# Kernel tuning notes

Measured on AMD Instinct MI355X. Metric: run time of the kernel, lower is better.

## Reference

```python
import jax, jax.numpy as jnp
import numpy as np

N_ITEMS = 100000
HIDDEN = 128
N_EDGES = 1600000


def setup_inputs() -> dict:
    key = jax.random.key(0)
    k1, k2, k3, k4 = jax.random.split(key, 4)
    item_emb = jax.random.normal(k1, (N_ITEMS, HIDDEN), dtype=jnp.float32) * 0.02
    adj_rows = jax.random.randint(k2, (N_EDGES,), 0, N_ITEMS, dtype=jnp.int32)
    adj_cols = jax.random.randint(k3, (N_EDGES,), 0, N_ITEMS, dtype=jnp.int32)
    adj_vals = jax.random.uniform(k4, (N_EDGES,), dtype=jnp.float32)
    return {
        "item_emb": item_emb,
        "adj_rows": adj_rows,
        "adj_cols": adj_cols,
        "adj_vals": adj_vals,
        "num_layers": 3,
    }


def _spmm(rows, cols, vals, embeds, n_rows):
    # y[r] = sum_{e: rows[e]==r} vals[e] * embeds[cols[e]]  (COO spmm)
    gathered = embeds[cols] * vals[:, None]  # [E, H]
    return jax.ops.segment_sum(gathered, rows, num_segments=n_rows)


def reference(item_emb, adj_rows, adj_cols, adj_vals, num_layers):
    embeds = [item_emb]
    for _ in range(num_layers):
        embeds.append(_spmm(adj_rows, adj_cols, adj_vals, embeds[-1], item_emb.shape[0]))
    # sum over all layer embeddings (running-sum aggregation)
    total = embeds[0]
    for e in embeds[1:]:
        total = total + e
    return (total, jnp.stack(embeds, axis=0))
```

## Files before the change

### kernel.cpp

```cpp
#include <hip/hip_runtime.h>
#include <hip/hip_fp16.h>

#define HIDDEN 128
#define SCAN_TILE 1024
#define SCAN_BLOCK 256

__global__ void zero_counts(int* __restrict__ counts, int n) {
    int i = blockIdx.x * blockDim.x + threadIdx.x;
    int stride = gridDim.x * blockDim.x;
    for (; i < n; i += stride) counts[i] = 0;
}

__global__ void hist_kernel(const int* __restrict__ rows, int* __restrict__ counts, int E) {
    int i = blockIdx.x * blockDim.x + threadIdx.x;
    int stride = gridDim.x * blockDim.x;
    for (; i < E; i += stride) atomicAdd(&counts[rows[i]], 1);
}

__global__ void scan_partial_sums(const int* __restrict__ counts,
                                  int* __restrict__ block_sums,
                                  int n) {
    __shared__ int sdata[SCAN_BLOCK];
    int t = threadIdx.x;
    int idx = blockIdx.x * SCAN_TILE + t * 4;
    int s = 0;
    if (idx + 3 < n) {
        int4 c = *reinterpret_cast<const int4*>(counts + idx);
        s = c.x + c.y + c.z + c.w;
    } else if (idx < n) {
        s = counts[idx];
        if (idx + 1 < n) s += counts[idx + 1];
        if (idx + 2 < n) s += counts[idx + 2];
    }
    sdata[t] = s;
    __syncthreads();
    for (int off = SCAN_BLOCK / 2; off > 0; off >>= 1) {
        if (t < off) sdata[t] += sdata[t + off];
        __syncthreads();
    }
    if (t == 0) block_sums[blockIdx.x] = sdata[0];
}

__global__ void scan_block_offsets(int* __restrict__ block_sums,
                                   int* __restrict__ row_ptr,
                                   int nb, int n) {
    __shared__ int sdata[SCAN_BLOCK];
    int t = threadIdx.x;
    int chunk = (nb + SCAN_BLOCK - 1) / SCAN_BLOCK;
    int lo = t * chunk;
    int hi = min(lo + chunk, nb);
    int s = 0;
    for (int i = lo; i < hi; ++i) s += block_sums[i];
    sdata[t] = s;
    __syncthreads();
    for (int off = 1; off < SCAN_BLOCK; off <<= 1) {
        int u = (t >= off) ? sdata[t - off] : 0;
        __syncthreads();
        sdata[t] += u;
        __syncthreads();
    }
    int run = sdata[t] - s;
    for (int i = lo; i < hi; ++i) {
        int v = block_sums[i];
        block_sums[i] = run;
        run += v;
    }
    if (t == SCAN_BLOCK - 1) row_ptr[n] = sdata[SCAN_BLOCK - 1];
}

__global__ void scan_apply(const int* counts,
                           const int* __restrict__ block_offsets,
                           int* __restrict__ row_ptr,
                           int* cursor,
                           int n) {
    __shared__ int sdata[SCAN_BLOCK];
    int t = threadIdx.x;
    int idx = blockIdx.x * SCAN_TILE + t * 4;
    int v0 = 0, v1 = 0, v2 = 0, v3 = 0;
    if (idx + 3 < n) {
        int4 c = *reinterpret_cast<const int4*>(counts + idx);
        v0 = c.x; v1 = c.y; v2 = c.z; v3 = c.w;
    } else if (idx < n) {
        v0 = counts[idx];
        if (idx + 1 < n) v1 = counts[idx + 1];
        if (idx + 2 < n) v2 = counts[idx + 2];
    }
    int s = v0 + v1 + v2 + v3;
    sdata[t] = s;
    __syncthreads();
    for (int off = 1; off < SCAN_BLOCK; off <<= 1) {
        int u = (t >= off) ? sdata[t - off] : 0;
        __syncthreads();
        sdata[t] += u;
        __syncthreads();
    }
    int run = sdata[t] - s + block_offsets[blockIdx.x];
    if (idx < n)     { row_ptr[idx]     = run; cursor[idx]     = run; run += v0; }
    if (idx + 1 < n) { row_ptr[idx + 1] = run; cursor[idx + 1] = run; run += v1; }
    if (idx + 2 < n) { row_ptr[idx + 2] = run; cursor[idx + 2] = run; run += v2; }
    if (idx + 3 < n) { row_ptr[idx + 3] = run; cursor[idx + 3] = run; run += v3; }
}

__global__ void scatter_kernel(const int* __restrict__ rows,
                               const int* __restrict__ cols,
                               const float* __restrict__ vals,
                               int* __restrict__ cursor,
                               int2* __restrict__ colval,
                               int E) {
    int i = blockIdx.x * blockDim.x + threadIdx.x;
    int stride = gridDim.x * blockDim.x;
    for (; i < E; i += stride) {
        int r = rows[i];
        int pos = atomicAdd(&cursor[r], 1);
        colval[pos] = make_int2(cols[i], __float_as_int(vals[i]));
    }
}

__global__ void convert_copy(const float4* __restrict__ src,
                             float4* __restrict__ s0,
                             float4* __restrict__ xh,
                             size_t n8) {
    size_t stride = (size_t)gridDim.x * blockDim.x;
    for (size_t i = (size_t)blockIdx.x * blockDim.x + threadIdx.x; i < n8; i += stride) {
        float4 a = src[i * 2];
        float4 b = src[i * 2 + 1];
        s0[i * 2]     = a;
        s0[i * 2 + 1] = b;
        __half2 h[4];
        h[0] = __floats2half2_rn(a.x, a.y);
        h[1] = __floats2half2_rn(a.z, a.w);
        h[2] = __floats2half2_rn(b.x, b.y);
        h[3] = __floats2half2_rn(b.z, b.w);
        xh[i] = *reinterpret_cast<float4*>(h);
    }
}

template <bool WRITE_SHADOW>
__global__ void spmm_h16(const int* __restrict__ row_ptr,
                         const int2* __restrict__ colval,
                         const float4* __restrict__ xh,
                         float* __restrict__ y,
                         float4* __restrict__ yh,
                         int n_rows) {
    int tid = (int)((size_t)blockIdx.x * blockDim.x + threadIdx.x);
    int row = tid >> 4;
    int li  = threadIdx.x & 15;
    if (row >= n_rows) return;

    int start = row_ptr[row];
    int end   = row_ptr[row + 1];

    float acc[8] = {0.f, 0.f, 0.f, 0.f, 0.f, 0.f, 0.f, 0.f};

    for (int base = start; base < end; base += 16) {
        int idx = base + li;
        int c = 0; float v = 0.f;
        if (idx < end) {
            int2 cv = colval[idx];
            c = cv.x;
            v = __int_as_float(cv.y);
        }
        int n = min(16, end - base);
        #pragma unroll 4
        for (int j = 0; j < n; ++j) {
            int   cj = __shfl(c, j, 16);
            float vj = __shfl(v, j, 16);
            float4 h4 = xh[(size_t)cj * 16 + li];
            const __half2* hp = reinterpret_cast<const __half2*>(&h4);
            float2 f0 = __half22float2(hp[0]);
            float2 f1 = __half22float2(hp[1]);
            float2 f2 = __half22float2(hp[2]);
            float2 f3 = __half22float2(hp[3]);
            acc[0] += vj * f0.x; acc[1] += vj * f0.y;
            acc[2] += vj * f1.x; acc[3] += vj * f1.y;
            acc[4] += vj * f2.x; acc[5] += vj * f2.y;
            acc[6] += vj * f3.x; acc[7] += vj * f3.y;
        }
    }

    size_t ob = (size_t)row * 32 + (size_t)(li * 2);
    ((float4*)y)[ob]     = make_float4(acc[0], acc[1], acc[2], acc[3]);
    ((float4*)y)[ob + 1] = make_float4(acc[4], acc[5], acc[6], acc[7]);

    if (WRITE_SHADOW) {
        __half2 h[4];
        h[0] = __floats2half2_rn(acc[0], acc[1]);
        h[1] = __floats2half2_rn(acc[2], acc[3]);
        h[2] = __floats2half2_rn(acc[4], acc[5]);
        h[3] = __floats2half2_rn(acc[6], acc[7]);
        yh[(size_t)row * 16 + li] = *reinterpret_cast<float4*>(h);
    }
}

__global__ void total_kernel(const float4* __restrict__ s0,
                             const float4* __restrict__ s1,
                             const float4* __restrict__ s2,
                             const float4* __restrict__ s3,
                             float4* __restrict__ t,
                             size_t n4) {
    size_t stride = (size_t)gridDim.x * blockDim.x;
    for (size_t i = (size_t)blockIdx.x * blockDim.x + threadIdx.x; i < n4; i += stride) {
        float4 a = s0[i], b = s1[i], c = s2[i], d = s3[i];
        float4 o;
        o.x = a.x + b.x + c.x + d.x;
        o.y = a.y + b.y + c.y + d.y;
        o.z = a.z + b.z + c.z + d.z;
        o.w = a.w + b.w + c.w + d.w;
        t[i] = o;
    }
}

extern "C" void kernel_launch(void* const* d_in, const int* in_sizes, int n_in,
                              void* d_out, int out_size, void* d_ws, size_t ws_size,
                              hipStream_t stream) {
    const float* item_emb = (const float*)d_in[0];
    const int*   adj_rows = (const int*)d_in[1];
    const int*   adj_cols = (const int*)d_in[2];
    const float* adj_vals = (const float*)d_in[3];

    const size_t NH = (size_t)in_sizes[0];
    const int    E  = in_sizes[1];
    const int    N  = (int)(NH / HIDDEN);

    float* T  = (float*)d_out;
    float* S0 = T + NH;
    float* S1 = S0 + NH;
    float* S2 = S1 + NH;
    float* S3 = S2 + NH;

    float4* shA = (float4*)T;
    float4* shB = (float4*)S3;

    char* ws = (char*)d_ws;
    int*   row_ptr = (int*)ws;                       ws += ((size_t)(N + 1) * 4 + 15) & ~15ull;
    int*   cursor  = (int*)ws;                       ws += ((size_t)N * 4 + 15) & ~15ull;
    int2*  colval  = (int2*)ws;

    const int nb = (N + SCAN_TILE - 1) / SCAN_TILE;
    int* block_sums = (int*)(colval + E) - nb;

    {
        int block = 256;
        int gridN = min((N + block - 1) / block, 4096);
        int gridE = min((E + block - 1) / block, 8192);
        zero_counts<<<gridN, block, 0, stream>>>(cursor, N);
        hist_kernel<<<gridE, block, 0, stream>>>(adj_rows, cursor, E);
        scan_partial_sums<<<nb, SCAN_BLOCK, 0, stream>>>(cursor, block_sums, N);
        scan_block_offsets<<<1, SCAN_BLOCK, 0, stream>>>(block_sums, row_ptr, nb, N);
        scan_apply<<<nb, SCAN_BLOCK, 0, stream>>>(cursor, block_sums, row_ptr, cursor, N);
        scatter_kernel<<<gridE, block, 0, stream>>>(adj_rows, adj_cols, adj_vals,
                                                    cursor, colval, E);
    }

    {
        size_t n8 = NH / 8;
        int block = 256;
        int grid = (int)min((n8 + block - 1) / block, (size_t)8192);
        convert_copy<<<grid, block, 0, stream>>>((const float4*)item_emb,
                                                 (float4*)S0, shA, n8);
    }

    {
        int block = 256;
        int grid = (N * 16 + block - 1) / block;
        spmm_h16<true><<<grid, block, 0, stream>>>(row_ptr, colval, shA, S1, shB, N);
        spmm_h16<true><<<grid, block, 0, stream>>>(row_ptr, colval, shB, S2, shA, N);
        spmm_h16<false><<<grid, block, 0, stream>>>(row_ptr, colval, shA, S3, nullptr, N);
    }

    {
        size_t n4 = NH / 4;
        int block = 256;
        int grid = (int)min((n4 + block - 1) / block, (size_t)8192);
        total_kernel<<<grid, block, 0, stream>>>((const float4*)S0, (const float4*)S1,
                                                 (const float4*)S2, (const float4*)S3,
                                                 (float4*)T, n4);
    }
}
```

Baseline: 698.5 us.

## Record histogram ranks to drop scatter atomics; use nontemporal loads/stores for streams

```diff
diff --git a/kernel.cpp b/kernel.cpp
--- a/kernel.cpp
+++ b/kernel.cpp
@@ -4,6 +4,17 @@
 #define HIDDEN 128
 #define SCAN_TILE 1024
 #define SCAN_BLOCK 256
+
+typedef float cvec4 __attribute__((ext_vector_type(4)));
+
+__device__ inline void nt_store4(float4* p, float4 v) {
+    cvec4 x; x.x = v.x; x.y = v.y; x.z = v.z; x.w = v.w;
+    __builtin_nontemporal_store(x, reinterpret_cast<cvec4*>(p));
+}
+__device__ inline float4 nt_load4(const float4* p) {
+    cvec4 x = __builtin_nontemporal_load(reinterpret_cast<const cvec4*>(p));
+    return make_float4(x.x, x.y, x.z, x.w);
+}
 
 __global__ void zero_counts(int* __restrict__ counts, int n) {
     int i = blockIdx.x * blockDim.x + threadIdx.x;
@@ -11,10 +22,13 @@
     for (; i < n; i += stride) counts[i] = 0;
 }
 
-__global__ void hist_kernel(const int* __restrict__ rows, int* __restrict__ counts, int E) {
+__global__ void hist_kernel(const int* __restrict__ rows,
+                            int* __restrict__ counts,
+                            int* __restrict__ rank,
+                            int E) {
     int i = blockIdx.x * blockDim.x + threadIdx.x;
     int stride = gridDim.x * blockDim.x;
-    for (; i < E; i += stride) atomicAdd(&counts[rows[i]], 1);
+    for (; i < E; i += stride) rank[i] = atomicAdd(&counts[rows[i]], 1);
 }
 
 __global__ void scan_partial_sums(const int* __restrict__ counts,
@@ -68,10 +82,9 @@
     if (t == SCAN_BLOCK - 1) row_ptr[n] = sdata[SCAN_BLOCK - 1];
 }
 
-__global__ void scan_apply(const int* counts,
+__global__ void scan_apply(const int* __restrict__ counts,
                            const int* __restrict__ block_offsets,
                            int* __restrict__ row_ptr,
-                           int* cursor,
                            int n) {
     __shared__ int sdata[SCAN_BLOCK];
     int t = threadIdx.x;
@@ -95,23 +108,23 @@
         __syncthreads();
     }
     int run = sdata[t] - s + block_offsets[blockIdx.x];
-    if (idx < n)     { row_ptr[idx]     = run; cursor[idx]     = run; run += v0; }
-    if (idx + 1 < n) { row_ptr[idx + 1] = run; cursor[idx + 1] = run; run += v1; }
-    if (idx + 2 < n) { row_ptr[idx + 2] = run; cursor[idx + 2] = run; run += v2; }
-    if (idx + 3 < n) { row_ptr[idx + 3] = run; cursor[idx + 3] = run; run += v3; }
+    if (idx < n)     { row_ptr[idx]     = run; run += v0; }
+    if (idx + 1 < n) { row_ptr[idx + 1] = run; run += v1; }
+    if (idx + 2 < n) { row_ptr[idx + 2] = run; run += v2; }
+    if (idx + 3 < n) { row_ptr[idx + 3] = run; run += v3; }
 }
 
 __global__ void scatter_kernel(const int* __restrict__ rows,
                                const int* __restrict__ cols,
                                const float* __restrict__ vals,
-                               int* __restrict__ cursor,
+                               const int* __restrict__ row_ptr,
+                               const int* __restrict__ rank,
                                int2* __restrict__ colval,
                                int E) {
     int i = blockIdx.x * blockDim.x + threadIdx.x;
     int stride = gridDim.x * blockDim.x;
     for (; i < E; i += stride) {
-        int r = rows[i];
-        int pos = atomicAdd(&cursor[r], 1);
+        int pos = row_ptr[rows[i]] + rank[i];
         colval[pos] = make_int2(cols[i], __float_as_int(vals[i]));
     }
 }
@@ -122,10 +135,10 @@
                              size_t n8) {
     size_t stride = (size_t)gridDim.x * blockDim.x;
     for (size_t i = (size_t)blockIdx.x * blockDim.x + threadIdx.x; i < n8; i += stride) {
-        float4 a = src[i * 2];
-        float4 b = src[i * 2 + 1];
-        s0[i * 2]     = a;
-        s0[i * 2 + 1] = b;
+        float4 a = nt_load4(src + i * 2);
+        float4 b = nt_load4(src + i * 2 + 1);
+        nt_store4(s0 + i * 2, a);
+        nt_store4(s0 + i * 2 + 1, b);
         __half2 h[4];
         h[0] = __floats2half2_rn(a.x, a.y);
         h[1] = __floats2half2_rn(a.z, a.w);
@@ -179,8 +192,8 @@
     }
 
     size_t ob = (size_t)row * 32 + (size_t)(li * 2);
-    ((float4*)y)[ob]     = make_float4(acc[0], acc[1], acc[2], acc[3]);
-    ((float4*)y)[ob + 1] = make_float4(acc[4], acc[5], acc[6], acc[7]);
+    nt_store4((float4*)y + ob,     make_float4(acc[0], acc[1], acc[2], acc[3]));
+    nt_store4((float4*)y + ob + 1, make_float4(acc[4], acc[5], acc[6], acc[7]));
 
     if (WRITE_SHADOW) {
         __half2 h[4];
@@ -200,13 +213,14 @@
                              size_t n4) {
     size_t stride = (size_t)gridDim.x * blockDim.x;
     for (size_t i = (size_t)blockIdx.x * blockDim.x + threadIdx.x; i < n4; i += stride) {
-        float4 a = s0[i], b = s1[i], c = s2[i], d = s3[i];
+        float4 a = nt_load4(s0 + i), b = nt_load4(s1 + i);
+        float4 c = nt_load4(s2 + i), d = nt_load4(s3 + i);
         float4 o;
         o.x = a.x + b.x + c.x + d.x;
         o.y = a.y + b.y + c.y + d.y;
         o.z = a.z + b.z + c.z + d.z;
         o.w = a.w + b.w + c.w + d.w;
-        t[i] = o;
+        nt_store4(t + i, o);
     }
 }
 
@@ -228,12 +242,13 @@
     float* S2 = S1 + NH;
     float* S3 = S2 + NH;
 
-    float4* shA = (float4*)T;
-    float4* shB = (float4*)S3;
+    float4* shA  = (float4*)T;
+    float4* shB  = (float4*)S3;
+    int*    rank = (int*)S1;
 
     char* ws = (char*)d_ws;
     int*   row_ptr = (int*)ws;                       ws += ((size_t)(N + 1) * 4 + 15) & ~15ull;
-    int*   cursor  = (int*)ws;                       ws += ((size_t)N * 4 + 15) & ~15ull;
+    int*   counts  = (int*)ws;                       ws += ((size_t)N * 4 + 15) & ~15ull;
     int2*  colval  = (int2*)ws;
 
     const int nb = (N + SCAN_TILE - 1) / SCAN_TILE;
@@ -243,13 +258,13 @@
         int block = 256;
         int gridN = min((N + block - 1) / block, 4096);
         int gridE = min((E + block - 1) / block, 8192);
-        zero_counts<<<gridN, block, 0, stream>>>(cursor, N);
-        hist_kernel<<<gridE, block, 0, stream>>>(adj_rows, cursor, E);
-        scan_partial_sums<<<nb, SCAN_BLOCK, 0, stream>>>(cursor, block_sums, N);
+        zero_counts<<<gridN, block, 0, stream>>>(counts, N);
+        hist_kernel<<<gridE, block, 0, stream>>>(adj_rows, counts, rank, E);
+        scan_partial_sums<<<nb, SCAN_BLOCK, 0, stream>>>(counts, block_sums, N);
         scan_block_offsets<<<1, SCAN_BLOCK, 0, stream>>>(block_sums, row_ptr, nb, N);
-        scan_apply<<<nb, SCAN_BLOCK, 0, stream>>>(cursor, block_sums, row_ptr, cursor, N);
+        scan_apply<<<nb, SCAN_BLOCK, 0, stream>>>(counts, block_sums, row_ptr, N);
         scatter_kernel<<<gridE, block, 0, stream>>>(adj_rows, adj_cols, adj_vals,
-                                                    cursor, colval, E);
+                                                    row_ptr, rank, colval, E);
     }
 
     {
```

Measured after the change: 634.9 us. 9.1% less time.
